# Kernel optimization log

Measured on AMD Instinct MI355X. Metric: run time of the kernel, lower is better.

## Reference

```python
import jax, jax.numpy as jnp
import numpy as np

DIM = 2048
N_HEADS = 16
N_KV_HEADS = 4
HEAD_DIM = DIM // N_HEADS  # 128
ROPE_BASE = 10000.0
B, S = 4, 2048


def rope_tables(seq_len, head_dim, base, dtype):
    half = head_dim // 2
    inv_freq = 1.0 / (base ** (jnp.arange(0, head_dim, 2, dtype=jnp.float32) / head_dim))
    t = jnp.arange(seq_len, dtype=jnp.float32)
    freqs = jnp.outer(t, inv_freq)  # [S, half]
    return jnp.cos(freqs).astype(dtype), jnp.sin(freqs).astype(dtype)


def apply_rotary(x, cos, sin):
    # x: [B, H, S, D]; cos/sin: [S, D/2] broadcast over B,H
    half = x.shape[-1] // 2
    x1, x2 = x[..., :half], x[..., half:]
    return jnp.concatenate((x1 * cos + x2 * sin, x1 * -sin + x2 * cos), axis=-1)


def setup_inputs() -> dict:
    key = jax.random.key(0)
    ks = jax.random.split(key, 5)
    sc = 1.0 / np.sqrt(DIM)
    return {
        "x": jax.random.normal(ks[0], (B, S, DIM), dtype=jnp.float32),
        "wq": jax.random.normal(ks[1], (DIM, DIM), dtype=jnp.float32) * sc,
        "wk": jax.random.normal(ks[2], (N_KV_HEADS * HEAD_DIM, DIM), dtype=jnp.float32) * sc,
        "wv": jax.random.normal(ks[3], (N_KV_HEADS * HEAD_DIM, DIM), dtype=jnp.float32) * sc,
        "wo": jax.random.normal(ks[4], (DIM, DIM), dtype=jnp.float32) * sc,
    }


def reference(x, wq, wk, wv, wo):
    bsz, seqlen, _ = x.shape
    q = jnp.einsum("bsd,ed->bse", x, wq).reshape(bsz, seqlen, N_HEADS, HEAD_DIM).transpose(0, 2, 1, 3)
    k = jnp.einsum("bsd,ed->bse", x, wk).reshape(bsz, seqlen, N_KV_HEADS, HEAD_DIM).transpose(0, 2, 1, 3)
    v = jnp.einsum("bsd,ed->bse", x, wv).reshape(bsz, seqlen, N_KV_HEADS, HEAD_DIM).transpose(0, 2, 1, 3)

    cos, sin = rope_tables(seqlen, HEAD_DIM, ROPE_BASE, q.dtype)
    q = apply_rotary(q, cos, sin)
    k = apply_rotary(k, cos, sin)

    rep = N_HEADS // N_KV_HEADS
    if rep > 1:
        k = jnp.repeat(k, rep, axis=1)
        v = jnp.repeat(v, rep, axis=1)

    scale = 1.0 / np.sqrt(HEAD_DIM)
    logits = jnp.einsum("bhqd,bhkd->bhqk", q, k) * scale
    causal = jnp.tril(jnp.ones((seqlen, seqlen), dtype=bool))
    logits = jnp.where(causal, logits, jnp.finfo(logits.dtype).min)
    attn = jax.nn.softmax(logits, axis=-1)
    y = jnp.einsum("bhqk,bhkd->bhqd", attn, v)

    y = y.transpose(0, 2, 1, 3).reshape(bsz, seqlen, DIM)
    return jnp.einsum("bsd,ed->bse", y, wo)
```

## Files before the change

### kernel.cpp

```cpp
#include <hip/hip_runtime.h>
#include <hip/hip_bf16.h>

typedef short s16x8 __attribute__((ext_vector_type(8)));
typedef float f32x4 __attribute__((ext_vector_type(4)));
typedef float f32x16 __attribute__((ext_vector_type(16)));
typedef unsigned u32;
typedef unsigned u32x4 __attribute__((ext_vector_type(4)));
typedef unsigned short u16;

#define DMODEL 2048
#define NH     16
#define NKV    4
#define HD     128
#define NB     4
#define SS     2048

static __device__ __forceinline__ u16 f2bf(float f) {
  unsigned u = __builtin_bit_cast(unsigned, f);
  u += 0x7fffu + ((u >> 16) & 1u);
  return (u16)(u >> 16);
}
static __device__ __forceinline__ float bf2f(u16 h) {
  unsigned u = ((unsigned)h) << 16;
  return __builtin_bit_cast(float, u);
}
static __device__ __forceinline__ u32 packbf(float a, float b) {
  return (u32)f2bf(a) | ((u32)f2bf(b) << 16);
}

typedef const __attribute__((address_space(1))) void* gas_p;
typedef __attribute__((address_space(3))) void* las_p;
#define GLOAD16(g, l) __builtin_amdgcn_global_load_lds((gas_p)(const void*)(g), (las_p)(void*)(l), 16, 0, 0)

__global__ void cast_all(const float* __restrict__ x,  const float* __restrict__ wq,
                         const float* __restrict__ wk, const float* __restrict__ wv,
                         const float* __restrict__ wo,
                         u16* __restrict__ xb, u16* __restrict__ wqkv, u16* __restrict__ wob)
{
  long gid = (long)blockIdx.x * 256 + threadIdx.x;
  long i = gid * 4;
  const float* src; u16* dst; long off;
  if (i < 16777216L)       { src = x;  dst = xb;             off = i; }
  else if (i < 20971520L)  { src = wq; dst = wqkv;           off = i - 16777216L; }
  else if (i < 22020096L)  { src = wk; dst = wqkv + 4194304; off = i - 20971520L; }
  else if (i < 23068672L)  { src = wv; dst = wqkv + 5242880; off = i - 22020096L; }
  else                     { src = wo; dst = wob;            off = i - 23068672L; }
  float4 v = *(const float4*)(src + off);
  ushort4 o;
  o.x = f2bf(v.x); o.y = f2bf(v.y); o.z = f2bf(v.z); o.w = f2bf(v.w);
  *(ushort4*)(dst + off) = o;
}

template<int NT, int EPI>
__global__ __launch_bounds__(512) void gemm256(
    const u16* __restrict__ A, const u16* __restrict__ Bm, int K,
    u16* __restrict__ Oq, u16* __restrict__ Ok, u16* __restrict__ Ov, float* __restrict__ Of)
{
  __shared__ __align__(16) u16 lds[2][32768];
  const int tid = threadIdx.x, l = tid & 63, w = tid >> 6;
  const int lg = l >> 4, lr = l & 15;
  const int wm = w >> 2, wn = w & 3;

  const int nwg = NT * 32;
  const int cpx = nwg >> 3;
  const int bid = blockIdx.x;
  const int swz = (bid & 7) * cpx + (bid >> 3);
  const int by = swz / NT, bx = swz % NT;
  const int rowBase = by * 256, colBase = bx * 256;

  const int rloc = w * 8 + (l >> 3);
  const int cgo  = ((l & 7) ^ (l >> 3)) * 8;
  const u16* gp[8];
#pragma unroll
  for (int seg = 0; seg < 8; seg++) {
    int half = (seg >> 1) & 1;
    int row  = (seg & 1) * 64 + rloc;
    if (seg < 4) gp[seg] = A  + (long)(rowBase + half * 128 + row) * K + cgo;
    else         gp[seg] = Bm + (long)(colBase + half * 128 + row) * K + cgo;
  }

  f32x4 acc[8][4] = {};

  auto stage = [&](int buf) {
    char* base = (char*)&lds[buf][0];
#pragma unroll
    for (int seg = 0; seg < 8; seg++)
      GLOAD16(gp[seg], base + seg * 8192 + w * 1024);
  };

  const int NKT = K >> 6;
  stage(0);
#pragma unroll
  for (int seg = 0; seg < 8; seg++) gp[seg] += 64;
  asm volatile("s_waitcnt vmcnt(0)" ::: "memory");
  __builtin_amdgcn_s_barrier();

  for (int kt = 0; kt < NKT; kt++) {
    const int cur = kt & 1;
    if (kt + 1 < NKT) {
      stage(cur ^ 1);
#pragma unroll
      for (int seg = 0; seg < 8; seg++) gp[seg] += 64;
      asm volatile("s_waitcnt vmcnt(8)" ::: "memory");
    } else {
      asm volatile("s_waitcnt vmcnt(0)" ::: "memory");
    }
    __builtin_amdgcn_s_barrier();
    asm volatile("" ::: "memory");

    const char* ab = (const char*)&lds[cur][0] + wm * 16384;
    const char* bb = (const char*)&lds[cur][0] + 32768 + (wn >> 1) * 16384;
    const int rbB = (wn & 1) * 64;
#pragma unroll
    for (int ks = 0; ks < 2; ks++) {
      const int c = ks * 4 + lg;
      s16x8 af[8], bfr[4];
#pragma unroll
      for (int m = 0; m < 8; m++) {
        int rr = m * 16 + lr;
        af[m] = *(const s16x8*)(ab + rr * 128 + ((c ^ (rr & 7)) * 16));
      }
#pragma unroll
      for (int n = 0; n < 4; n++) {
        int rb = rbB + n * 16 + lr;
        bfr[n] = *(const s16x8*)(bb + rb * 128 + ((c ^ (rb & 7)) * 16));
      }
      __builtin_amdgcn_s_setprio(1);
#pragma unroll
      for (int m = 0; m < 8; m++)
#pragma unroll
        for (int n = 0; n < 4; n++)
          acc[m][n] = __builtin_amdgcn_mfma_f32_16x16x32_bf16(af[m], bfr[n], acc[m][n], 0, 0, 0);
      __builtin_amdgcn_s_setprio(0);
    }
    asm volatile("" ::: "memory");
    __builtin_amdgcn_s_barrier();
    asm volatile("" ::: "memory");
  }

#pragma unroll
  for (int m = 0; m < 8; m++)
#pragma unroll
    for (int n = 0; n < 4; n++)
#pragma unroll
      for (int r = 0; r < 4; r++) {
        int row = rowBase + wm * 128 + m * 16 + lg * 4 + r;
        int col = colBase + wn * 64 + n * 16 + lr;
        float v = acc[m][n][r];
        if (EPI == 0) {
          int b = row >> 11, s = row & 2047;
          u16 hv = f2bf(v);
          if (col < 2048) {
            int hh = col >> 7, d = col & 127;
            Oq[(((long)(b * NH + hh)) * SS + s) * HD + d] = hv;
          } else if (col < 2560) {
            int c2 = col - 2048, kh = c2 >> 7, d = c2 & 127;
            Ok[(((long)(b * NKV + kh)) * SS + s) * HD + d] = hv;
          } else {
            int c2 = col - 2560, kh = c2 >> 7, d = c2 & 127;
            Ov[(((long)(b * NKV + kh)) * HD + d) * SS + s] = hv;
          }
        } else {
          Of[(long)row * DMODEL + col] = v;
        }
      }
}

__global__ void rope_kernel(u16* __restrict__ Qr, u16* __restrict__ Kr)
{
  long gid = (long)blockIdx.x * 256 + threadIdx.x;
  int i = (int)(gid & 63);
  long row = gid >> 6;
  int s;
  u16* p;
  const long qrows = (long)NB * NH * SS;
  if (row < qrows) { s = (int)(row & 2047); p = Qr + row * HD; }
  else             { long r2 = row - qrows; s = (int)(r2 & 2047); p = Kr + r2 * HD; }
  float inv = exp2f(-(float)i * 0.20762050593046015f);
  float fr = (float)s * inv;
  float c = cosf(fr), sn = sinf(fr);
  float x1 = bf2f(p[i]), x2 = bf2f(p[i + 64]);
  p[i]      = f2bf(x1 * c + x2 * sn);
  p[i + 64] = f2bf(-x1 * sn + x2 * c);
}

__global__ __launch_bounds__(512) void attn_fwd(const u16* __restrict__ Qr, const u16* __restrict__ Kr,
                                                const u16* __restrict__ Vt, u16* __restrict__ Y)
{
  __shared__ __align__(16) u16 Ks[2][64 * 128];
  __shared__ __align__(16) u16 Vs[2][128 * 64];

  const int tid = threadIdx.x, l = tid & 63, w = tid >> 6;
  const int lq = l & 31, hi = l >> 5;
  const int p = blockIdx.x, h = blockIdx.y, b = blockIdx.z;
  const int kvh = h >> 2;

  const u16* Kh = Kr + ((long)(b * NKV + kvh)) * SS * HD;
  const u16* Vh = Vt + ((long)(b * NKV + kvh)) * HD * SS;
  const float scale = 0.08838834764831845f;

  auto stageK = [&](int buf, int kvb) {
    char* kb = (char*)&Ks[buf][0];
#pragma unroll
    for (int i = 0; i < 2; i++) {
      int L = w * 2048 + i * 1024 + l * 16;
      int r = L >> 8;
      int cl = (L >> 4) & 15;
      int cg = (cl & 8) | ((cl ^ r) & 7);
      GLOAD16((const char*)(Kh + (long)(kvb + r) * HD) + cg * 16, kb + w * 2048 + i * 1024);
    }
  };
  auto stageV = [&](int buf, int kvb) {
    char* vb = (char*)&Vs[buf][0];
#pragma unroll
    for (int i = 0; i < 2; i++) {
      int L = w * 2048 + i * 1024 + l * 16;
      int r = L >> 7;
      int cl = (L >> 4) & 7;
      int cg = (cl ^ r) & 7;
      GLOAD16((const char*)(Vh + (long)r * SS + kvb) + cg * 16, vb + w * 2048 + i * 1024);
    }
  };

  for (int job = 0; job < 2; job++) {
    const int qt = job ? p : 7 - p;
    const int qRow0 = qt * 256 + w * 32;
    const int qMax = qRow0 + 31;
    const int nT = 4 * qt + 4;
    const int myq = qRow0 + lq;
    const u16* Qh = Qr + (((long)(b * NH + h)) * SS + qRow0) * HD;
    u16* Yh = Y + ((long)b * SS) * DMODEL + h * HD;

    s16x8 qf[8];
#pragma unroll
    for (int kk = 0; kk < 8; kk++)
      qf[kk] = *(const s16x8*)(Qh + (long)lq * HD + kk * 16 + hi * 8);

    float m_run = -1e30f, l_run = 0.f;
    f32x16 oacc[4] = {};

    stageK(0, 0); stageV(0, 0);

    for (int t = 0; t < nT; t++) {
      const int cur = t & 1;
      if (t + 1 < nT) {
        stageK(cur ^ 1, (t + 1) * 64);
        stageV(cur ^ 1, (t + 1) * 64);
        asm volatile("s_waitcnt vmcnt(4)" ::: "memory");
      } else {
        asm volatile("s_waitcnt vmcnt(0)" ::: "memory");
      }
      __builtin_amdgcn_s_barrier();
      asm volatile("" ::: "memory");

      if (t * 64 <= qMax) {
        const char* kb = (const char*)&Ks[cur][0];
        const char* vb = (const char*)&Vs[cur][0];
        f32x16 sacc[2] = {};
#pragma unroll
        for (int kk = 0; kk < 8; kk++) {
          int ch = kk * 2 + hi;
#pragma unroll
          for (int tile = 0; tile < 2; tile++) {
            int rr = tile * 32 + lq;
            int cs = (ch & 8) | ((ch ^ rr) & 7);
            s16x8 kf = *(const s16x8*)(kb + rr * 256 + cs * 16);
            sacc[tile] = __builtin_amdgcn_mfma_f32_32x32x16_bf16(kf, qf[kk], sacc[tile], 0, 0, 0);
          }
        }
        const bool full = (t * 64 + 63 <= qRow0);
        float pmax = -1e30f;
#pragma unroll
        for (int tile = 0; tile < 2; tile++)
#pragma unroll
          for (int r = 0; r < 16; r++) {
            int kv = t * 64 + tile * 32 + (r & 3) + 8 * (r >> 2) + 4 * hi;
            float v = sacc[tile][r] * scale;
            if (!full && kv > myq) v = -30000.f;
            sacc[tile][r] = v;
            pmax = fmaxf(pmax, v);
          }
        pmax = fmaxf(pmax, __shfl_xor(pmax, 32));
        if (!__all(pmax - m_run <= 8.0f)) {
          float mnew = fmaxf(m_run, pmax);
          float sf = __expf(m_run - mnew);
          m_run = mnew; l_run *= sf;
          int sfi = __builtin_bit_cast(int, sf);
#pragma unroll
          for (int r = 0; r < 16; r++) {
            int qq = (r & 3) + 8 * (r >> 2) + 4 * hi;
            float sfr = __builtin_bit_cast(float, __builtin_amdgcn_ds_bpermute(qq << 2, sfi));
#pragma unroll
            for (int n = 0; n < 4; n++) oacc[n][r] *= sfr;
          }
        }
        float rs = 0.f;
#pragma unroll
        for (int tile = 0; tile < 2; tile++)
#pragma unroll
          for (int r = 0; r < 16; r++) {
            float pv = __expf(sacc[tile][r] - m_run);
            sacc[tile][r] = pv;
            rs += pv;
          }
        rs += __shfl_xor(rs, 32);
        l_run += rs;
        s16x8 pav[4];
#pragma unroll
        for (int tile = 0; tile < 2; tile++) {
          u32 qk[8], sw[8];
#pragma unroll
          for (int j = 0; j < 8; j++) {
            qk[j] = packbf(sacc[tile][2 * j], sacc[tile][2 * j + 1]);
            sw[j] = __shfl_xor(qk[j], 32);
          }
          u32x4 f0, f1;
          f0[0] = hi ? sw[2] : qk[0];
          f0[1] = hi ? sw[3] : qk[1];
          f0[2] = hi ? qk[2] : sw[0];
          f0[3] = hi ? qk[3] : sw[1];
          f1[0] = hi ? sw[6] : qk[4];
          f1[1] = hi ? sw[7] : qk[5];
          f1[2] = hi ? qk[6] : sw[4];
          f1[3] = hi ? qk[7] : sw[5];
          pav[tile * 2 + 0] = __builtin_bit_cast(s16x8, f0);
          pav[tile * 2 + 1] = __builtin_bit_cast(s16x8, f1);
        }
#pragma unroll
        for (int n = 0; n < 4; n++) {
          int rr = n * 32 + lq;
#pragma unroll
          for (int kk = 0; kk < 4; kk++) {
            int ch = kk * 2 + hi;
            int cs = (ch ^ rr) & 7;
            s16x8 vf = *(const s16x8*)(vb + rr * 128 + cs * 16);
            oacc[n] = __builtin_amdgcn_mfma_f32_32x32x16_bf16(pav[kk], vf, oacc[n], 0, 0, 0);
          }
        }
      }
      asm volatile("" ::: "memory");
      __builtin_amdgcn_s_barrier();
      asm volatile("" ::: "memory");
    }

    float linv = 1.f / l_run;
    int li = __builtin_bit_cast(int, linv);
#pragma unroll
    for (int r = 0; r < 16; r++) {
      int qq = (r & 3) + 8 * (r >> 2) + 4 * hi;
      float lr_ = __builtin_bit_cast(float, __builtin_amdgcn_ds_bpermute(qq << 2, li));
      u16* yrow = Yh + (long)(qRow0 + qq) * DMODEL;
#pragma unroll
      for (int n = 0; n < 4; n++)
        yrow[n * 32 + lq] = f2bf(oacc[n][r] * lr_);
    }
  }
}

extern "C" void kernel_launch(void* const* d_in, const int* in_sizes, int n_in,
                              void* d_out, int out_size, void* d_ws, size_t ws_size,
                              hipStream_t stream) {
  const float* x  = (const float*)d_in[0];
  const float* wq = (const float*)d_in[1];
  const float* wk = (const float*)d_in[2];
  const float* wv = (const float*)d_in[3];
  const float* wo = (const float*)d_in[4];
  float* out = (float*)d_out;
  char* ws = (char*)d_ws;

  u16* Xb   = (u16*)ws;
  u16* Wqkv = (u16*)(ws + 33554432);
  u16* Wob  = (u16*)(ws + 46137344);
  u16* Qr   = (u16*)(ws + 54525952);
  u16* Kr   = (u16*)(ws + 88080384);
  u16* Vt   = (u16*)(ws + 96468992);
  u16* Y    = Xb;

  cast_all<<<26624, 256, 0, stream>>>(x, wq, wk, wv, wo, Xb, Wqkv, Wob);
  gemm256<12, 0><<<384, 512, 0, stream>>>(Xb, Wqkv, DMODEL, Qr, Kr, Vt, nullptr);
  rope_kernel<<<40960, 256, 0, stream>>>(Qr, Kr);
  dim3 ag(4, NH, NB);
  attn_fwd<<<ag, 512, 0, stream>>>(Qr, Kr, Vt, Y);
  gemm256<8, 1><<<256, 512, 0, stream>>>(Y, Wob, DMODEL, nullptr, nullptr, nullptr, out);
}
```

Before: 378.3 us.

## Interleave next-tile global loads with MFMA phases in GEMM main loop

Restructures the GEMM k-loop into four phases over row quarters. Each phase issues part of the next tile's global-to-LDS loads, then loads A fragments and runs its MFMAs, so memory traffic is spread across the compute instead of issued in one burst before it. B fragments are loaded once per tile for both k-substeps. This adds more barriers per tile and makes the vmcnt wait bookkeeping more delicate, which risks stalls or wrong synchronization.

Result: faster. 370.5 us (-2.0%).

```diff
diff --git a/kernel.cpp b/kernel.cpp
--- a/kernel.cpp
+++ b/kernel.cpp
@@ -51,6 +51,32 @@
   *(ushort4*)(dst + off) = o;
 }
 
+#define GPHASE(MQ, STG, WAIT)                                               \
+  {                                                                         \
+    s16x8 af[2][2];                                                         \
+    _Pragma("unroll") for (int j = 0; j < 2; j++)                           \
+      _Pragma("unroll") for (int ks = 0; ks < 2; ks++) {                    \
+        int rr = (MQ) * 32 + j * 16 + lr;                                   \
+        int c = ks * 4 + lg;                                                \
+        af[j][ks] = *(const s16x8*)(ab + rr * 128 + ((c ^ (rr & 7)) * 16)); \
+      }                                                                     \
+    STG;                                                                    \
+    WAIT;                                                                   \
+    asm volatile("" ::: "memory");                                          \
+    __builtin_amdgcn_s_barrier();                                           \
+    asm volatile("" ::: "memory");                                          \
+    __builtin_amdgcn_s_setprio(1);                                          \
+    _Pragma("unroll") for (int ks = 0; ks < 2; ks++)                        \
+      _Pragma("unroll") for (int j = 0; j < 2; j++)                         \
+        _Pragma("unroll") for (int n = 0; n < 4; n++)                       \
+          acc[(MQ) * 2 + j][n] = __builtin_amdgcn_mfma_f32_16x16x32_bf16(   \
+              af[j][ks], bfr[n][ks], acc[(MQ) * 2 + j][n], 0, 0, 0);        \
+    __builtin_amdgcn_s_setprio(0);                                          \
+    asm volatile("" ::: "memory");                                          \
+    __builtin_amdgcn_s_barrier();                                           \
+    asm volatile("" ::: "memory");                                          \
+  }
+
 template<int NT, int EPI>
 __global__ __launch_bounds__(512) void gemm256(
     const u16* __restrict__ A, const u16* __restrict__ Bm, int K,
@@ -81,61 +107,58 @@
 
   f32x4 acc[8][4] = {};
 
-  auto stage = [&](int buf) {
-    char* base = (char*)&lds[buf][0];
+  const int NKT = K >> 6;
+  {
+    char* nb = (char*)&lds[0][0];
 #pragma unroll
     for (int seg = 0; seg < 8; seg++)
-      GLOAD16(gp[seg], base + seg * 8192 + w * 1024);
-  };
-
-  const int NKT = K >> 6;
-  stage(0);
-#pragma unroll
-  for (int seg = 0; seg < 8; seg++) gp[seg] += 64;
-  asm volatile("s_waitcnt vmcnt(0)" ::: "memory");
-  __builtin_amdgcn_s_barrier();
+      GLOAD16(gp[seg], nb + seg * 8192 + w * 1024);
+#pragma unroll
+    for (int seg = 0; seg < 8; seg++) gp[seg] += 64;
+    asm volatile("s_waitcnt vmcnt(0)" ::: "memory");
+    __builtin_amdgcn_s_barrier();
+    asm volatile("" ::: "memory");
+  }
 
   for (int kt = 0; kt < NKT; kt++) {
     const int cur = kt & 1;
-    if (kt + 1 < NKT) {
-      stage(cur ^ 1);
-#pragma unroll
-      for (int seg = 0; seg < 8; seg++) gp[seg] += 64;
-      asm volatile("s_waitcnt vmcnt(8)" ::: "memory");
-    } else {
-      asm volatile("s_waitcnt vmcnt(0)" ::: "memory");
-    }
-    __builtin_amdgcn_s_barrier();
-    asm volatile("" ::: "memory");
-
+    const bool pre = (kt + 1 < NKT);
     const char* ab = (const char*)&lds[cur][0] + wm * 16384;
     const char* bb = (const char*)&lds[cur][0] + 32768 + (wn >> 1) * 16384;
+    char* nb = (char*)&lds[cur ^ 1][0];
     const int rbB = (wn & 1) * 64;
-#pragma unroll
-    for (int ks = 0; ks < 2; ks++) {
-      const int c = ks * 4 + lg;
-      s16x8 af[8], bfr[4];
-#pragma unroll
-      for (int m = 0; m < 8; m++) {
-        int rr = m * 16 + lr;
-        af[m] = *(const s16x8*)(ab + rr * 128 + ((c ^ (rr & 7)) * 16));
+
+    s16x8 bfr[4][2];
+#pragma unroll
+    for (int n = 0; n < 4; n++)
+#pragma unroll
+      for (int ks = 0; ks < 2; ks++) {
+        int rb = rbB + n * 16 + lr;
+        int c = ks * 4 + lg;
+        bfr[n][ks] = *(const s16x8*)(bb + rb * 128 + ((c ^ (rb & 7)) * 16));
       }
-#pragma unroll
-      for (int n = 0; n < 4; n++) {
-        int rb = rbB + n * 16 + lr;
-        bfr[n] = *(const s16x8*)(bb + rb * 128 + ((c ^ (rb & 7)) * 16));
-      }
-      __builtin_amdgcn_s_setprio(1);
-#pragma unroll
-      for (int m = 0; m < 8; m++)
-#pragma unroll
-        for (int n = 0; n < 4; n++)
-          acc[m][n] = __builtin_amdgcn_mfma_f32_16x16x32_bf16(af[m], bfr[n], acc[m][n], 0, 0, 0);
-      __builtin_amdgcn_s_setprio(0);
+    GPHASE(0,
+      { if (pre) { GLOAD16(gp[4], nb + 4 * 8192 + w * 1024);
+                   GLOAD16(gp[5], nb + 5 * 8192 + w * 1024); } },
+      { });
+    GPHASE(1,
+      { if (pre) { GLOAD16(gp[6], nb + 6 * 8192 + w * 1024);
+                   GLOAD16(gp[7], nb + 7 * 8192 + w * 1024); } },
+      { if (pre) { asm volatile("s_waitcnt vmcnt(4)" ::: "memory"); }
+        else     { asm volatile("s_waitcnt vmcnt(0)" ::: "memory"); } });
+    GPHASE(2,
+      { if (pre) { GLOAD16(gp[0], nb + 0 * 8192 + w * 1024);
+                   GLOAD16(gp[2], nb + 2 * 8192 + w * 1024); } },
+      { });
+    GPHASE(3,
+      { if (pre) { GLOAD16(gp[1], nb + 1 * 8192 + w * 1024);
+                   GLOAD16(gp[3], nb + 3 * 8192 + w * 1024); } },
+      { if (pre) { asm volatile("s_waitcnt vmcnt(2)" ::: "memory"); } });
+
+    if (pre) {
+#pragma unroll
+      for (int seg = 0; seg < 8; seg++) gp[seg] += 64;
     }
-    asm volatile("" ::: "memory");
-    __builtin_amdgcn_s_barrier();
-    asm volatile("" ::: "memory");
   }
 
 #pragma unroll
```
